# Performance work log

Hardware: AMD Instinct MI355X
Metric: run time of the kernel (lower is better)

The kernel has to match this reference:

```python
import jax, jax.numpy as jnp
import numpy as np

BS, DIM, N_CLASSES = 4096, 512, 100
POS_W, NEG_W = 2.0, 40.0
MARGIN, POS_T, NEG_T = 0.1, 0.5, 0.5


def setup_inputs() -> dict:
    key = jax.random.key(0)
    k1, k2 = jax.random.split(key)
    x = jax.random.normal(k1, (BS, DIM), dtype=jnp.float32)
    x = x / jnp.linalg.norm(x, axis=-1, keepdims=True)  # cosine-mode embeddings
    labels = jax.random.randint(k2, (BS,), 0, N_CLASSES, dtype=jnp.int64 if jax.config.jax_enable_x64 else jnp.int32)
    return {"batch": x, "labels": labels}


def _masked_logsumexp(sims, mask, use_max):
    # Faithful port of Criterion.masked_logsumexp with dim=0 (per-column).
    m = sims * mask  # bool mask promotes; masked-out entries become 0
    ref = jnp.max(m, axis=0) if use_max else jnp.min(m, axis=0)  # (BS,)
    ref = jax.lax.stop_gradient(ref)
    nz = (jnp.max(m, axis=0) + jnp.min(m, axis=0)) != 0  # columns with any nonzero masked entry
    s = jnp.sum(jnp.exp(sims - ref[None, :]) * mask, axis=0)  # (BS,)
    vals = jnp.log(jnp.where(nz, s, 1.0)) + ref
    return vals, nz


def _masked_mean_softplus(vals, nz, w):
    cnt = jnp.sum(nz).astype(vals.dtype)
    sp = jax.nn.softplus(vals) / w
    mean = jnp.sum(jnp.where(nz, sp, 0.0)) / jnp.maximum(cnt, 1.0)
    # torch path returns scalar 0 from masked_logsumexp when no nz columns -> softplus(0)/w
    return jnp.where(cnt > 0, mean, jax.nn.softplus(0.0) / w)


def reference(batch, labels):
    sim = batch @ batch.T                                  # (BS, BS) cosine similarity
    same = labels[:, None] == labels[None, :]
    diff = ~same
    eye = jnp.eye(sim.shape[0], dtype=bool)

    # per-row bounds: hardest positive (min sim, excl. self) / hardest negative (max sim)
    pos_bound = jnp.min(jnp.where(same & ~eye, sim, jnp.inf), axis=1)   # (BS,)
    neg_bound = jnp.max(jnp.where(diff, sim, -jnp.inf), axis=1)        # (BS,)

    # torch broadcasting applies bounds per-COLUMN (last dim)
    neg_mask = diff & (sim + MARGIN > pos_bound[None, :])
    pos_mask = same & (sim - MARGIN < neg_bound[None, :])

    w_pos = -POS_W * (sim - POS_T)
    w_neg = NEG_W * (sim - NEG_T)

    pos_vals, pos_nz = _masked_logsumexp(w_pos, pos_mask, use_max=False)
    neg_vals, neg_nz = _masked_logsumexp(w_neg, neg_mask, use_max=True)

    loss = _masked_mean_softplus(pos_vals, pos_nz, POS_W) \
         + _masked_mean_softplus(neg_vals, neg_nz, NEG_W)
    return loss
```

## Files before the change

### kernel.cpp

```cpp
#include <hip/hip_runtime.h>
#include <stdint.h>


#define BS 4096
#define DIM 512
#define NTILES 528

typedef __attribute__((ext_vector_type(8))) short short8;
typedef __attribute__((ext_vector_type(4))) float f32x4;

#define TILE_USH (128 * 64)

__device__ __forceinline__ unsigned fenc(float f){
  unsigned u = __float_as_uint(f);
  return (u & 0x80000000u) ? ~u : (u | 0x80000000u);
}
__device__ __forceinline__ float fdec(unsigned e){
  unsigned u = (e & 0x80000000u) ? (e & 0x7fffffffu) : ~e;
  return __uint_as_float(u);
}
__device__ __forceinline__ ushort f2bf(float f){
  unsigned u = __float_as_uint(f);
  return (ushort)((u + 0x7fffu + ((u >> 16) & 1u)) >> 16);
}
__device__ __forceinline__ void gld_lds16(void* ldsp, const void* gp){
  __builtin_amdgcn_global_load_lds((const __attribute__((address_space(1))) void*)gp,
                                   (__attribute__((address_space(3))) void*)ldsp, 16, 0, 0);
}

__global__ void k_convert(const float* __restrict__ x, ushort* __restrict__ xh){
  int i = blockIdx.x * blockDim.x + threadIdx.x;
  float4 v = ((const float4*)x)[i];
  ((ushort4*)xh)[i] = make_ushort4(f2bf(v.x), f2bf(v.y), f2bf(v.z), f2bf(v.w));
}

__device__ __forceinline__ void gemm_tile(f32x4 (&acc)[4][4], ushort* lds,
                                          const ushort* __restrict__ Xh,
                                          int Rm, int Rn, int t)
{
  const int l  = t & 63;
  const int w  = t >> 6;
  const int wm = w >> 1, wn = w & 1;
  const int lc = l & 15;
  const int lq = l >> 4;
  const int r0 = t >> 3;
  const int gx = (t & 7) ^ (r0 & 7);
  const int lds_i = t * 8;

  #pragma unroll
  for (int i = 0; i < 4; ++i)
    #pragma unroll
    for (int j = 0; j < 4; ++j) acc[i][j] = (f32x4){0.f, 0.f, 0.f, 0.f};

  for (int ks = 0; ks < 8; ++ks){
    const int kb = ks * 64 + gx * 8;
    #pragma unroll
    for (int rep = 0; rep < 4; ++rep){
      const int row = rep * 32 + r0;
      const int lo  = rep * 2048 + lds_i;
      gld_lds16(&lds[lo],            Xh + (size_t)(Rm + row) * DIM + kb);
      gld_lds16(&lds[TILE_USH + lo], Xh + (size_t)(Rn + row) * DIM + kb);
    }
    __syncthreads();
    #pragma unroll
    for (int kk = 0; kk < 2; ++kk){
      const int gr = kk * 4 + lq;
      const int sl = (gr ^ (l & 7)) * 8;
      short8 ah[4], bh[4];
      #pragma unroll
      for (int f = 0; f < 4; ++f){
        ah[f] = *(const short8*)&lds[(wm * 64 + f * 16 + lc) * 64 + sl];
        bh[f] = *(const short8*)&lds[TILE_USH + (wn * 64 + f * 16 + lc) * 64 + sl];
      }
      #pragma unroll
      for (int fm = 0; fm < 4; ++fm)
        #pragma unroll
        for (int fn = 0; fn < 4; ++fn)
          acc[fm][fn] = __builtin_amdgcn_mfma_f32_16x16x32_bf16(ah[fm], bh[fn], acc[fm][fn], 0, 0, 0);
    }
    __syncthreads();
  }
}

__device__ __forceinline__ void epi_bounds(const f32x4 (&acc)[4][4],
    const int* __restrict__ labels, const int (&labr)[4][4],
    unsigned* pos_enc, unsigned* neg_enc,
    int Rm, int Rn, bool diag, int t)
{
  const int l  = t & 63;
  const int w  = t >> 6;
  const int wm = w >> 1, wn = w & 1;
  const int lc = l & 15, lq = l >> 4;
  const int crow0 = Rm + wm * 64;
  const int ccol0 = Rn + wn * 64;
  const float INF = __builtin_inff();

  #pragma unroll
  for (int fm = 0; fm < 4; ++fm){
    float mn[4] = {INF, INF, INF, INF};
    float mx[4] = {-INF, -INF, -INF, -INF};
    #pragma unroll
    for (int fn = 0; fn < 4; ++fn){
      const int gc = ccol0 + fn * 16 + lc;
      const int labc = labels[gc];
      #pragma unroll
      for (int v = 0; v < 4; ++v){
        const float s = acc[fm][fn][v];
        const int grow = crow0 + fm * 16 + lq * 4 + v;
        const bool same = (labc == labr[fm][v]);
        mn[v] = fminf(mn[v], (same && (grow != gc)) ? s : INF);
        mx[v] = fmaxf(mx[v], same ? -INF : s);
      }
    }
    #pragma unroll
    for (int off = 1; off < 16; off <<= 1)
      #pragma unroll
      for (int v = 0; v < 4; ++v){
        mn[v] = fminf(mn[v], __shfl_xor(mn[v], off));
        mx[v] = fmaxf(mx[v], __shfl_xor(mx[v], off));
      }
    if (lc == 0){
      #pragma unroll
      for (int v = 0; v < 4; ++v){
        const int grow = crow0 + fm * 16 + lq * 4 + v;
        if (mn[v] < INF)  atomicMin(&pos_enc[grow], fenc(mn[v]));
        if (mx[v] > -INF) atomicMax(&neg_enc[grow], fenc(mx[v]));
      }
    }
  }
  if (!diag){
    #pragma unroll
    for (int fn = 0; fn < 4; ++fn){
      const int gc = ccol0 + fn * 16 + lc;
      const int labc = labels[gc];
      float mn = INF, mx = -INF;
      #pragma unroll
      for (int fm = 0; fm < 4; ++fm)
        #pragma unroll
        for (int v = 0; v < 4; ++v){
          const float s = acc[fm][fn][v];
          const bool same = (labc == labr[fm][v]);
          mn = fminf(mn, same ? s : INF);
          mx = fmaxf(mx, same ? -INF : s);
        }
      #pragma unroll
      for (int off = 16; off < 64; off <<= 1){
        mn = fminf(mn, __shfl_xor(mn, off));
        mx = fmaxf(mx, __shfl_xor(mx, off));
      }
      if (l < 16){
        if (mn < INF)  atomicMin(&pos_enc[gc], fenc(mn));
        if (mx > -INF) atomicMax(&neg_enc[gc], fenc(mx));
      }
    }
  }
}

template<bool AB>
__device__ __forceinline__ unsigned rd_enc(unsigned* p){
  if (AB) return __hip_atomic_load(p, __ATOMIC_RELAXED, __HIP_MEMORY_SCOPE_AGENT);
  return *p;
}

template<bool AB>
__device__ __forceinline__ void epi_stats(const f32x4 (&acc)[4][4],
    const int* __restrict__ labels, const int (&labr)[4][4],
    unsigned* pos_enc, unsigned* neg_enc,
    unsigned* maxN_enc, unsigned* minN_enc, float* SN,
    unsigned* maxP_enc, unsigned* minP_enc, float* SP,
    int Rm, int Rn, bool diag, int t)
{
  const int l  = t & 63;
  const int w  = t >> 6;
  const int wm = w >> 1, wn = w & 1;
  const int lc = l & 15, lq = l >> 4;
  const int crow0 = Rm + wm * 64;
  const int ccol0 = Rn + wn * 64;
  const float INF = __builtin_inff();

  #pragma unroll
  for (int fn = 0; fn < 4; ++fn){
    const int gc = ccol0 + fn * 16 + lc;
    const int labc = labels[gc];
    const unsigned pe = rd_enc<AB>(&pos_enc[gc]);
    const float pb = (pe == 0xFFFFFFFFu) ? INF : fdec(pe);
    const unsigned ne = rd_enc<AB>(&neg_enc[gc]);
    const float nb = (ne == 0u) ? -INF : fdec(ne);
    float mxN = -INF, mnN = INF, sN = 0.f;
    float mxP = -INF, mnP = INF, sP = 0.f;
    #pragma unroll
    for (int fm = 0; fm < 4; ++fm)
      #pragma unroll
      for (int v = 0; v < 4; ++v){
        const float s = acc[fm][fn][v];
        const bool same = (labc == labr[fm][v]);
        const float wN = 40.0f * (s - 0.5f);
        const bool mN = (!same) && (s + 0.1f > pb);
        const float mvN = mN ? wN : 0.0f;
        mxN = fmaxf(mxN, mvN); mnN = fminf(mnN, mvN);
        sN += mN ? __expf(wN) : 0.0f;
        const float wP = -2.0f * (s - 0.5f);
        const bool mP = same && (s - 0.1f < nb);
        const float mvP = mP ? wP : 0.0f;
        mxP = fmaxf(mxP, mvP); mnP = fminf(mnP, mvP);
        sP += mP ? __expf(wP) : 0.0f;
      }
    #pragma unroll
    for (int off = 16; off < 64; off <<= 1){
      mxN = fmaxf(mxN, __shfl_xor(mxN, off));
      mnN = fminf(mnN, __shfl_xor(mnN, off));
      sN += __shfl_xor(sN, off);
      mxP = fmaxf(mxP, __shfl_xor(mxP, off));
      mnP = fminf(mnP, __shfl_xor(mnP, off));
      sP += __shfl_xor(sP, off);
    }
    if (l < 16){
      atomicMax(&maxN_enc[gc], fenc(mxN));
      atomicMin(&minN_enc[gc], fenc(mnN));
      atomicAdd(&SN[gc], sN);
      atomicMax(&maxP_enc[gc], fenc(mxP));
      atomicMin(&minP_enc[gc], fenc(mnP));
      atomicAdd(&SP[gc], sP);
    }
  }
  if (!diag){
    #pragma unroll
    for (int fm = 0; fm < 4; ++fm){
      float pbr[4], nbr[4];
      #pragma unroll
      for (int v = 0; v < 4; ++v){
        const int grow = crow0 + fm * 16 + lq * 4 + v;
        const unsigned pe = rd_enc<AB>(&pos_enc[grow]);
        pbr[v] = (pe == 0xFFFFFFFFu) ? INF : fdec(pe);
        const unsigned ne = rd_enc<AB>(&neg_enc[grow]);
        nbr[v] = (ne == 0u) ? -INF : fdec(ne);
      }
      float mxN[4], mnN[4], sN[4], mxP[4], mnP[4], sP[4];
      #pragma unroll
      for (int v = 0; v < 4; ++v){
        mxN[v] = -INF; mnN[v] = INF; sN[v] = 0.f;
        mxP[v] = -INF; mnP[v] = INF; sP[v] = 0.f;
      }
      #pragma unroll
      for (int fn = 0; fn < 4; ++fn){
        const int gc = ccol0 + fn * 16 + lc;
        const int labc = labels[gc];
        #pragma unroll
        for (int v = 0; v < 4; ++v){
          const float s = acc[fm][fn][v];
          const bool same = (labc == labr[fm][v]);
          const float wN = 40.0f * (s - 0.5f);
          const bool mN = (!same) && (s + 0.1f > pbr[v]);
          const float mvN = mN ? wN : 0.0f;
          mxN[v] = fmaxf(mxN[v], mvN); mnN[v] = fminf(mnN[v], mvN);
          sN[v] += mN ? __expf(wN) : 0.0f;
          const float wP = -2.0f * (s - 0.5f);
          const bool mP = same && (s - 0.1f < nbr[v]);
          const float mvP = mP ? wP : 0.0f;
          mxP[v] = fmaxf(mxP[v], mvP); mnP[v] = fminf(mnP[v], mvP);
          sP[v] += mP ? __expf(wP) : 0.0f;
        }
      }
      #pragma unroll
      for (int off = 1; off < 16; off <<= 1)
        #pragma unroll
        for (int v = 0; v < 4; ++v){
          mxN[v] = fmaxf(mxN[v], __shfl_xor(mxN[v], off));
          mnN[v] = fminf(mnN[v], __shfl_xor(mnN[v], off));
          sN[v] += __shfl_xor(sN[v], off);
          mxP[v] = fmaxf(mxP[v], __shfl_xor(mxP[v], off));
          mnP[v] = fminf(mnP[v], __shfl_xor(mnP[v], off));
          sP[v] += __shfl_xor(sP[v], off);
        }
      if (lc == 0){
        #pragma unroll
        for (int v = 0; v < 4; ++v){
          const int grow = crow0 + fm * 16 + lq * 4 + v;
          atomicMax(&maxN_enc[grow], fenc(mxN[v]));
          atomicMin(&minN_enc[grow], fenc(mnN[v]));
          atomicAdd(&SN[grow], sN[v]);
          atomicMax(&maxP_enc[grow], fenc(mxP[v]));
          atomicMin(&minP_enc[grow], fenc(mnP[v]));
          atomicAdd(&SP[grow], sP[v]);
        }
      }
    }
  }
}

__device__ __forceinline__ void decode_tile(int bid, int& Rm, int& Rn, bool& diag){
  int wg = (bid & 7) * 66 + (bid >> 3);
  int ii = wg, bm = 0;
  while (ii >= 32 - bm){ ii -= 32 - bm; ++bm; }
  const int bn = bm + ii;
  diag = (bm == bn);
  Rm = bm * 128; Rn = bn * 128;
}

__global__ __launch_bounds__(256, 3)
void k_fused(const ushort* __restrict__ Xh, const int* __restrict__ labels,
             unsigned* pos_enc, unsigned* neg_enc,
             unsigned* maxN_enc, unsigned* minN_enc, float* SN,
             unsigned* maxP_enc, unsigned* minP_enc, float* SP,
             unsigned* bar)
{
  __shared__ ushort lds[2 * TILE_USH];
  const int t = threadIdx.x;
  int Rm, Rn; bool diag;
  decode_tile((int)blockIdx.x, Rm, Rn, diag);

  f32x4 acc[4][4];
  gemm_tile(acc, lds, Xh, Rm, Rn, t);

  const int wm = (t >> 6) >> 1, lq = (t & 63) >> 4;
  int labr[4][4];
  #pragma unroll
  for (int fm = 0; fm < 4; ++fm)
    #pragma unroll
    for (int v = 0; v < 4; ++v)
      labr[fm][v] = labels[Rm + wm * 64 + fm * 16 + lq * 4 + v];

  epi_bounds(acc, labels, labr, pos_enc, neg_enc, Rm, Rn, diag, t);

  __syncthreads();
  if (t == 0){
    __threadfence();
    __hip_atomic_fetch_add(bar, 1u, __ATOMIC_ACQ_REL, __HIP_MEMORY_SCOPE_AGENT);
    unsigned spins = 0;
    while (__hip_atomic_load(bar, __ATOMIC_ACQUIRE, __HIP_MEMORY_SCOPE_AGENT) < (unsigned)NTILES
           && ++spins < 20000000u)
      __builtin_amdgcn_s_sleep(8);
  }
  __syncthreads();

  epi_stats<true>(acc, labels, labr, pos_enc, neg_enc,
                  maxN_enc, minN_enc, SN, maxP_enc, minP_enc, SP, Rm, Rn, diag, t);
}

template<int PHASE>
__global__ __launch_bounds__(256)
void k_gemm(const ushort* __restrict__ Xh, const int* __restrict__ labels,
            unsigned* pos_enc, unsigned* neg_enc,
            unsigned* maxN_enc, unsigned* minN_enc, float* SN,
            unsigned* maxP_enc, unsigned* minP_enc, float* SP)
{
  __shared__ ushort lds[2 * TILE_USH];
  const int t = threadIdx.x;
  int Rm, Rn; bool diag;
  decode_tile((int)blockIdx.x, Rm, Rn, diag);

  f32x4 acc[4][4];
  gemm_tile(acc, lds, Xh, Rm, Rn, t);

  const int wm = (t >> 6) >> 1, lq = (t & 63) >> 4;
  int labr[4][4];
  #pragma unroll
  for (int fm = 0; fm < 4; ++fm)
    #pragma unroll
    for (int v = 0; v < 4; ++v)
      labr[fm][v] = labels[Rm + wm * 64 + fm * 16 + lq * 4 + v];

  if (PHASE == 1)
    epi_bounds(acc, labels, labr, pos_enc, neg_enc, Rm, Rn, diag, t);
  else
    epi_stats<false>(acc, labels, labr, pos_enc, neg_enc,
                     maxN_enc, minN_enc, SN, maxP_enc, minP_enc, SP, Rm, Rn, diag, t);
}

__global__ void k_finalize(const unsigned* __restrict__ maxN_enc, const unsigned* __restrict__ minN_enc,
                           const float* __restrict__ SN,
                           const unsigned* __restrict__ maxP_enc, const unsigned* __restrict__ minP_enc,
                           const float* __restrict__ SP, float* __restrict__ out)
{
  const int t = threadIdx.x;
  float sumP = 0.f, cP = 0.f, sumN = 0.f, cN = 0.f;
  #pragma unroll
  for (int i = 0; i < 4; ++i){
    const int c = t + i * 1024;
    const float mxN = fdec(maxN_enc[c]), mnN = fdec(minN_enc[c]);
    if (mxN + mnN != 0.0f){ sumN += log1pf(SN[c]); cN += 1.0f; }
    const float mxP = fdec(maxP_enc[c]), mnP = fdec(minP_enc[c]);
    if (mxP + mnP != 0.0f){ sumP += log1pf(SP[c]); cP += 1.0f; }
  }
  #pragma unroll
  for (int off = 32; off; off >>= 1){
    sumP += __shfl_down(sumP, off); cP += __shfl_down(cP, off);
    sumN += __shfl_down(sumN, off); cN += __shfl_down(cN, off);
  }
  __shared__ float red[16][4];
  const int w = t >> 6;
  if ((t & 63) == 0){ red[w][0] = sumP; red[w][1] = cP; red[w][2] = sumN; red[w][3] = cN; }
  __syncthreads();
  if (t == 0){
    float SPs = 0.f, CPs = 0.f, SNs = 0.f, CNs = 0.f;
    for (int i = 0; i < 16; ++i){ SPs += red[i][0]; CPs += red[i][1]; SNs += red[i][2]; CNs += red[i][3]; }
    const float LN2 = 0.69314718055994531f;
    const float tP = (CPs > 0.f) ? (SPs / 2.0f)  / fmaxf(CPs, 1.f) : LN2 / 2.0f;
    const float tN = (CNs > 0.f) ? (SNs / 40.0f) / fmaxf(CNs, 1.f) : LN2 / 40.0f;
    out[0] = tP + tN;
  }
}

extern "C" void kernel_launch(void* const* d_in, const int* in_sizes, int n_in,
                              void* d_out, int out_size, void* d_ws, size_t ws_size,
                              hipStream_t stream) {
  const float* x    = (const float*)d_in[0];
  const int* labels = (const int*)d_in[1];
  char* W = (char*)d_ws;
  ushort* Xh = (ushort*)W;
  char* Z = W + (4u << 20);
  unsigned* neg_enc  = (unsigned*)(Z + 0 * 16384);
  unsigned* maxN_enc = (unsigned*)(Z + 1 * 16384);
  unsigned* maxP_enc = (unsigned*)(Z + 2 * 16384);
  float*    SN       = (float*)   (Z + 3 * 16384);
  float*    SP       = (float*)   (Z + 4 * 16384);
  unsigned* bar      = (unsigned*)(Z + 5 * 16384);
  char* F = Z + 6 * 16384;
  unsigned* pos_enc  = (unsigned*)(F + 0 * 16384);
  unsigned* minN_enc = (unsigned*)(F + 1 * 16384);
  unsigned* minP_enc = (unsigned*)(F + 2 * 16384);

  hipMemsetAsync(Z, 0x00, 6 * 16384, stream);
  hipMemsetAsync(F, 0xFF, 3 * 16384, stream);
  k_convert<<<(BS * DIM / 4) / 256, 256, 0, stream>>>(x, Xh);

  int nb = 0, ncu = 0;
  hipDeviceProp_t prop;
  int dev = 0;
  hipGetDevice(&dev);
  if (hipGetDeviceProperties(&prop, dev) == hipSuccess) ncu = prop.multiProcessorCount;
  bool fused = (hipOccupancyMaxActiveBlocksPerMultiprocessor(&nb, k_fused, 256, 0) == hipSuccess)
               && (ncu > 0) && ((long)nb * ncu >= NTILES);

  if (fused){
    k_fused<<<NTILES, 256, 0, stream>>>(Xh, labels, pos_enc, neg_enc,
                                        maxN_enc, minN_enc, SN, maxP_enc, minP_enc, SP, bar);
  } else {
    k_gemm<1><<<NTILES, 256, 0, stream>>>(Xh, labels, pos_enc, neg_enc,
                                          maxN_enc, minN_enc, SN, maxP_enc, minP_enc, SP);
    k_gemm<2><<<NTILES, 256, 0, stream>>>(Xh, labels, pos_enc, neg_enc,
                                          maxN_enc, minN_enc, SN, maxP_enc, minP_enc, SP);
  }
  k_finalize<<<1, 1024, 0, stream>>>(maxN_enc, minN_enc, SN, maxP_enc, minP_enc, SP, (float*)d_out);
}
```

Baseline: 185.6 us.

## Replace atomics and grid barrier with per-tile partial buffers and separate reduction kernels

```diff
diff --git a/kernel.cpp b/kernel.cpp
--- a/kernel.cpp
+++ b/kernel.cpp
@@ -5,20 +5,13 @@
 #define BS 4096
 #define DIM 512
 #define NTILES 528
+#define NSLOT 32
 
 typedef __attribute__((ext_vector_type(8))) short short8;
 typedef __attribute__((ext_vector_type(4))) float f32x4;
 
 #define TILE_USH (128 * 64)
 
-__device__ __forceinline__ unsigned fenc(float f){
-  unsigned u = __float_as_uint(f);
-  return (u & 0x80000000u) ? ~u : (u | 0x80000000u);
-}
-__device__ __forceinline__ float fdec(unsigned e){
-  unsigned u = (e & 0x80000000u) ? (e & 0x7fffffffu) : ~e;
-  return __uint_as_float(u);
-}
 __device__ __forceinline__ ushort f2bf(float f){
   unsigned u = __float_as_uint(f);
   return (ushort)((u + 0x7fffu + ((u >> 16) & 1u)) >> 16);
@@ -32,6 +25,15 @@
   int i = blockIdx.x * blockDim.x + threadIdx.x;
   float4 v = ((const float4*)x)[i];
   ((ushort4*)xh)[i] = make_ushort4(f2bf(v.x), f2bf(v.y), f2bf(v.z), f2bf(v.w));
+}
+
+__device__ __forceinline__ void decode_tile(int bid, int& Rm, int& Rn, bool& diag){
+  int wg = (bid & 7) * 66 + (bid >> 3);
+  int ii = wg, bm = 0;
+  while (ii >= 32 - bm){ ii -= 32 - bm; ++bm; }
+  const int bn = bm + ii;
+  diag = (bm == bn);
+  Rm = bm * 128; Rn = bn * 128;
 }
 
 __device__ __forceinline__ void gemm_tile(f32x4 (&acc)[4][4], ushort* lds,
@@ -82,18 +84,36 @@
   }
 }
 
-__device__ __forceinline__ void epi_bounds(const f32x4 (&acc)[4][4],
-    const int* __restrict__ labels, const int (&labr)[4][4],
-    unsigned* pos_enc, unsigned* neg_enc,
-    int Rm, int Rn, bool diag, int t)
+__global__ __launch_bounds__(256)
+void k_bounds(const ushort* __restrict__ Xh, const int* __restrict__ labels,
+              float* __restrict__ posB, float* __restrict__ negB)
 {
+  __shared__ ushort lds[2 * TILE_USH];
+  const int t = threadIdx.x;
+  int Rm, Rn; bool diag;
+  decode_tile((int)blockIdx.x, Rm, Rn, diag);
+  const int bm = Rm >> 7, bn = Rn >> 7;
+
+  f32x4 acc[4][4];
+  gemm_tile(acc, lds, Xh, Rm, Rn, t);
+
   const int l  = t & 63;
   const int w  = t >> 6;
   const int wm = w >> 1, wn = w & 1;
   const int lc = l & 15, lq = l >> 4;
-  const int crow0 = Rm + wm * 64;
-  const int ccol0 = Rn + wn * 64;
   const float INF = __builtin_inff();
+
+  int labr[4][4];
+  #pragma unroll
+  for (int fm = 0; fm < 4; ++fm)
+    #pragma unroll
+    for (int v = 0; v < 4; ++v)
+      labr[fm][v] = labels[Rm + wm * 64 + fm * 16 + lq * 4 + v];
+
+  float* sMnS = (float*)lds;
+  float* sMxS = sMnS + 256;
+  float* sMnT = sMnS + 512;
+  float* sMxT = sMnS + 768;
 
   #pragma unroll
   for (int fm = 0; fm < 4; ++fm){
@@ -101,12 +121,12 @@
     float mx[4] = {-INF, -INF, -INF, -INF};
     #pragma unroll
     for (int fn = 0; fn < 4; ++fn){
-      const int gc = ccol0 + fn * 16 + lc;
+      const int gc = Rn + wn * 64 + fn * 16 + lc;
       const int labc = labels[gc];
       #pragma unroll
       for (int v = 0; v < 4; ++v){
         const float s = acc[fm][fn][v];
-        const int grow = crow0 + fm * 16 + lq * 4 + v;
+        const int grow = Rm + wm * 64 + fm * 16 + lq * 4 + v;
         const bool same = (labc == labr[fm][v]);
         mn[v] = fminf(mn[v], (same && (grow != gc)) ? s : INF);
         mx[v] = fmaxf(mx[v], same ? -INF : s);
@@ -122,16 +142,16 @@
     if (lc == 0){
       #pragma unroll
       for (int v = 0; v < 4; ++v){
-        const int grow = crow0 + fm * 16 + lq * 4 + v;
-        if (mn[v] < INF)  atomicMin(&pos_enc[grow], fenc(mn[v]));
-        if (mx[v] > -INF) atomicMax(&neg_enc[grow], fenc(mx[v]));
+        const int r64 = fm * 16 + lq * 4 + v;
+        sMnS[(wm * 2 + wn) * 64 + r64] = mn[v];
+        sMxS[(wm * 2 + wn) * 64 + r64] = mx[v];
       }
     }
   }
   if (!diag){
     #pragma unroll
     for (int fn = 0; fn < 4; ++fn){
-      const int gc = ccol0 + fn * 16 + lc;
+      const int gc = Rn + wn * 64 + fn * 16 + lc;
       const int labc = labels[gc];
       float mn = INF, mx = -INF;
       #pragma unroll
@@ -149,170 +169,56 @@
         mx = fmaxf(mx, __shfl_xor(mx, off));
       }
       if (l < 16){
-        if (mn < INF)  atomicMin(&pos_enc[gc], fenc(mn));
-        if (mx > -INF) atomicMax(&neg_enc[gc], fenc(mx));
-      }
-    }
-  }
-}
-
-template<bool AB>
-__device__ __forceinline__ unsigned rd_enc(unsigned* p){
-  if (AB) return __hip_atomic_load(p, __ATOMIC_RELAXED, __HIP_MEMORY_SCOPE_AGENT);
-  return *p;
-}
-
-template<bool AB>
-__device__ __forceinline__ void epi_stats(const f32x4 (&acc)[4][4],
-    const int* __restrict__ labels, const int (&labr)[4][4],
-    unsigned* pos_enc, unsigned* neg_enc,
-    unsigned* maxN_enc, unsigned* minN_enc, float* SN,
-    unsigned* maxP_enc, unsigned* minP_enc, float* SP,
-    int Rm, int Rn, bool diag, int t)
-{
-  const int l  = t & 63;
-  const int w  = t >> 6;
-  const int wm = w >> 1, wn = w & 1;
-  const int lc = l & 15, lq = l >> 4;
-  const int crow0 = Rm + wm * 64;
-  const int ccol0 = Rn + wn * 64;
-  const float INF = __builtin_inff();
-
-  #pragma unroll
-  for (int fn = 0; fn < 4; ++fn){
-    const int gc = ccol0 + fn * 16 + lc;
-    const int labc = labels[gc];
-    const unsigned pe = rd_enc<AB>(&pos_enc[gc]);
-    const float pb = (pe == 0xFFFFFFFFu) ? INF : fdec(pe);
-    const unsigned ne = rd_enc<AB>(&neg_enc[gc]);
-    const float nb = (ne == 0u) ? -INF : fdec(ne);
-    float mxN = -INF, mnN = INF, sN = 0.f;
-    float mxP = -INF, mnP = INF, sP = 0.f;
-    #pragma unroll
-    for (int fm = 0; fm < 4; ++fm)
-      #pragma unroll
-      for (int v = 0; v < 4; ++v){
-        const float s = acc[fm][fn][v];
-        const bool same = (labc == labr[fm][v]);
-        const float wN = 40.0f * (s - 0.5f);
-        const bool mN = (!same) && (s + 0.1f > pb);
-        const float mvN = mN ? wN : 0.0f;
-        mxN = fmaxf(mxN, mvN); mnN = fminf(mnN, mvN);
-        sN += mN ? __expf(wN) : 0.0f;
-        const float wP = -2.0f * (s - 0.5f);
-        const bool mP = same && (s - 0.1f < nb);
-        const float mvP = mP ? wP : 0.0f;
-        mxP = fmaxf(mxP, mvP); mnP = fminf(mnP, mvP);
-        sP += mP ? __expf(wP) : 0.0f;
-      }
-    #pragma unroll
-    for (int off = 16; off < 64; off <<= 1){
-      mxN = fmaxf(mxN, __shfl_xor(mxN, off));
-      mnN = fminf(mnN, __shfl_xor(mnN, off));
-      sN += __shfl_xor(sN, off);
-      mxP = fmaxf(mxP, __shfl_xor(mxP, off));
-      mnP = fminf(mnP, __shfl_xor(mnP, off));
-      sP += __shfl_xor(sP, off);
-    }
-    if (l < 16){
-      atomicMax(&maxN_enc[gc], fenc(mxN));
-      atomicMin(&minN_enc[gc], fenc(mnN));
-      atomicAdd(&SN[gc], sN);
-      atomicMax(&maxP_enc[gc], fenc(mxP));
-      atomicMin(&minP_enc[gc], fenc(mnP));
-      atomicAdd(&SP[gc], sP);
-    }
-  }
-  if (!diag){
-    #pragma unroll
-    for (int fm = 0; fm < 4; ++fm){
-      float pbr[4], nbr[4];
-      #pragma unroll
-      for (int v = 0; v < 4; ++v){
-        const int grow = crow0 + fm * 16 + lq * 4 + v;
-        const unsigned pe = rd_enc<AB>(&pos_enc[grow]);
-        pbr[v] = (pe == 0xFFFFFFFFu) ? INF : fdec(pe);
-        const unsigned ne = rd_enc<AB>(&neg_enc[grow]);
-        nbr[v] = (ne == 0u) ? -INF : fdec(ne);
-      }
-      float mxN[4], mnN[4], sN[4], mxP[4], mnP[4], sP[4];
-      #pragma unroll
-      for (int v = 0; v < 4; ++v){
-        mxN[v] = -INF; mnN[v] = INF; sN[v] = 0.f;
-        mxP[v] = -INF; mnP[v] = INF; sP[v] = 0.f;
-      }
-      #pragma unroll
-      for (int fn = 0; fn < 4; ++fn){
-        const int gc = ccol0 + fn * 16 + lc;
-        const int labc = labels[gc];
-        #pragma unroll
-        for (int v = 0; v < 4; ++v){
-          const float s = acc[fm][fn][v];
-          const bool same = (labc == labr[fm][v]);
-          const float wN = 40.0f * (s - 0.5f);
-          const bool mN = (!same) && (s + 0.1f > pbr[v]);
-          const float mvN = mN ? wN : 0.0f;
-          mxN[v] = fmaxf(mxN[v], mvN); mnN[v] = fminf(mnN[v], mvN);
-          sN[v] += mN ? __expf(wN) : 0.0f;
-          const float wP = -2.0f * (s - 0.5f);
-          const bool mP = same && (s - 0.1f < nbr[v]);
-          const float mvP = mP ? wP : 0.0f;
-          mxP[v] = fmaxf(mxP[v], mvP); mnP[v] = fminf(mnP[v], mvP);
-          sP[v] += mP ? __expf(wP) : 0.0f;
-        }
-      }
-      #pragma unroll
-      for (int off = 1; off < 16; off <<= 1)
-        #pragma unroll
-        for (int v = 0; v < 4; ++v){
-          mxN[v] = fmaxf(mxN[v], __shfl_xor(mxN[v], off));
-          mnN[v] = fminf(mnN[v], __shfl_xor(mnN[v], off));
-          sN[v] += __shfl_xor(sN[v], off);
-          mxP[v] = fmaxf(mxP[v], __shfl_xor(mxP[v], off));
-          mnP[v] = fminf(mnP[v], __shfl_xor(mnP[v], off));
-          sP[v] += __shfl_xor(sP[v], off);
-        }
-      if (lc == 0){
-        #pragma unroll
-        for (int v = 0; v < 4; ++v){
-          const int grow = crow0 + fm * 16 + lq * 4 + v;
-          atomicMax(&maxN_enc[grow], fenc(mxN[v]));
-          atomicMin(&minN_enc[grow], fenc(mnN[v]));
-          atomicAdd(&SN[grow], sN[v]);
-          atomicMax(&maxP_enc[grow], fenc(mxP[v]));
-          atomicMin(&minP_enc[grow], fenc(mnP[v]));
-          atomicAdd(&SP[grow], sP[v]);
-        }
-      }
-    }
-  }
-}
-
-__device__ __forceinline__ void decode_tile(int bid, int& Rm, int& Rn, bool& diag){
-  int wg = (bid & 7) * 66 + (bid >> 3);
-  int ii = wg, bm = 0;
-  while (ii >= 32 - bm){ ii -= 32 - bm; ++bm; }
-  const int bn = bm + ii;
-  diag = (bm == bn);
-  Rm = bm * 128; Rn = bn * 128;
-}
-
-__global__ __launch_bounds__(256, 3)
-void k_fused(const ushort* __restrict__ Xh, const int* __restrict__ labels,
-             unsigned* pos_enc, unsigned* neg_enc,
-             unsigned* maxN_enc, unsigned* minN_enc, float* SN,
-             unsigned* maxP_enc, unsigned* minP_enc, float* SP,
-             unsigned* bar)
+        const int c64 = fn * 16 + lc;
+        sMnT[(wn * 2 + wm) * 64 + c64] = mn;
+        sMxT[(wn * 2 + wm) * 64 + c64] = mx;
+      }
+    }
+  }
+  __syncthreads();
+  if (t < 128){
+    const int h = t >> 6, r = t & 63;
+    posB[(size_t)bn * BS + Rm + t] = fminf(sMnS[(h * 2 + 0) * 64 + r], sMnS[(h * 2 + 1) * 64 + r]);
+    negB[(size_t)bn * BS + Rm + t] = fmaxf(sMxS[(h * 2 + 0) * 64 + r], sMxS[(h * 2 + 1) * 64 + r]);
+    if (!diag){
+      posB[(size_t)bm * BS + Rn + t] = fminf(sMnT[(h * 2 + 0) * 64 + r], sMnT[(h * 2 + 1) * 64 + r]);
+      negB[(size_t)bm * BS + Rn + t] = fmaxf(sMxT[(h * 2 + 0) * 64 + r], sMxT[(h * 2 + 1) * 64 + r]);
+    }
+  }
+}
+
+__global__ void k_redbounds(const float* __restrict__ posB, const float* __restrict__ negB,
+                            float* __restrict__ pos_bound, float* __restrict__ neg_bound){
+  const int r = blockIdx.x * 256 + threadIdx.x;
+  float mn = __builtin_inff(), mx = -__builtin_inff();
+  #pragma unroll
+  for (int s = 0; s < NSLOT; ++s){
+    mn = fminf(mn, posB[(size_t)s * BS + r]);
+    mx = fmaxf(mx, negB[(size_t)s * BS + r]);
+  }
+  pos_bound[r] = mn;
+  neg_bound[r] = mx;
+}
+
+__global__ __launch_bounds__(256)
+void k_stats(const ushort* __restrict__ Xh, const int* __restrict__ labels,
+             const float* __restrict__ pos_bound, const float* __restrict__ neg_bound,
+             float* __restrict__ SNp, float* __restrict__ SPp)
 {
   __shared__ ushort lds[2 * TILE_USH];
   const int t = threadIdx.x;
   int Rm, Rn; bool diag;
   decode_tile((int)blockIdx.x, Rm, Rn, diag);
+  const int bm = Rm >> 7, bn = Rn >> 7;
 
   f32x4 acc[4][4];
   gemm_tile(acc, lds, Xh, Rm, Rn, t);
 
-  const int wm = (t >> 6) >> 1, lq = (t & 63) >> 4;
+  const int l  = t & 63;
+  const int w  = t >> 6;
+  const int wm = w >> 1, wn = w & 1;
+  const int lc = l & 15, lq = l >> 4;
+
   int labr[4][4];
   #pragma unroll
   for (int fm = 0; fm < 4; ++fm)
@@ -320,67 +226,106 @@
     for (int v = 0; v < 4; ++v)
       labr[fm][v] = labels[Rm + wm * 64 + fm * 16 + lq * 4 + v];
 
-  epi_bounds(acc, labels, labr, pos_enc, neg_enc, Rm, Rn, diag, t);
-
+  float* sSNs = (float*)lds;
+  float* sSPs = sSNs + 256;
+  float* sSNt = sSNs + 512;
+  float* sSPt = sSNs + 768;
+
+  #pragma unroll
+  for (int fn = 0; fn < 4; ++fn){
+    const int gc = Rn + wn * 64 + fn * 16 + lc;
+    const int labc = labels[gc];
+    const float pb = pos_bound[gc];
+    const float nb = neg_bound[gc];
+    float sN = 0.f, sP = 0.f;
+    #pragma unroll
+    for (int fm = 0; fm < 4; ++fm)
+      #pragma unroll
+      for (int v = 0; v < 4; ++v){
+        const float s = acc[fm][fn][v];
+        const bool same = (labc == labr[fm][v]);
+        sN += ((!same) && (s + 0.1f > pb)) ? __expf(40.0f * (s - 0.5f)) : 0.0f;
+        sP += (same && (s - 0.1f < nb))    ? __expf(-2.0f * (s - 0.5f)) : 0.0f;
+      }
+    #pragma unroll
+    for (int off = 16; off < 64; off <<= 1){
+      sN += __shfl_xor(sN, off);
+      sP += __shfl_xor(sP, off);
+    }
+    if (l < 16){
+      const int c64 = fn * 16 + lc;
+      sSNs[(wn * 2 + wm) * 64 + c64] = sN;
+      sSPs[(wn * 2 + wm) * 64 + c64] = sP;
+    }
+  }
+  if (!diag){
+    #pragma unroll
+    for (int fm = 0; fm < 4; ++fm){
+      float pbr[4], nbr[4];
+      #pragma unroll
+      for (int v = 0; v < 4; ++v){
+        const int grow = Rm + wm * 64 + fm * 16 + lq * 4 + v;
+        pbr[v] = pos_bound[grow];
+        nbr[v] = neg_bound[grow];
+      }
+      float sN[4] = {0.f, 0.f, 0.f, 0.f}, sP[4] = {0.f, 0.f, 0.f, 0.f};
+      #pragma unroll
+      for (int fn = 0; fn < 4; ++fn){
+        const int gc = Rn + wn * 64 + fn * 16 + lc;
+        const int labc = labels[gc];
+        #pragma unroll
+        for (int v = 0; v < 4; ++v){
+          const float s = acc[fm][fn][v];
+          const bool same = (labc == labr[fm][v]);
+          sN[v] += ((!same) && (s + 0.1f > pbr[v])) ? __expf(40.0f * (s - 0.5f)) : 0.0f;
+          sP[v] += (same && (s - 0.1f < nbr[v]))    ? __expf(-2.0f * (s - 0.5f)) : 0.0f;
+        }
+      }
+      #pragma unroll
+      for (int off = 1; off < 16; off <<= 1)
+        #pragma unroll
+        for (int v = 0; v < 4; ++v){
+          sN[v] += __shfl_xor(sN[v], off);
+          sP[v] += __shfl_xor(sP[v], off);
+        }
+      if (lc == 0){
+        #pragma unroll
+        for (int v = 0; v < 4; ++v){
+          const int r64 = fm * 16 + lq * 4 + v;
+          sSNt[(wm * 2 + wn) * 64 + r64] = sN[v];
+          sSPt[(wm * 2 + wn) * 64 + r64] = sP[v];
+        }
+      }
+    }
+  }
   __syncthreads();
-  if (t == 0){
-    __threadfence();
-    __hip_atomic_fetch_add(bar, 1u, __ATOMIC_ACQ_REL, __HIP_MEMORY_SCOPE_AGENT);
-    unsigned spins = 0;
-    while (__hip_atomic_load(bar, __ATOMIC_ACQUIRE, __HIP_MEMORY_SCOPE_AGENT) < (unsigned)NTILES
-           && ++spins < 20000000u)
-      __builtin_amdgcn_s_sleep(8);
-  }
-  __syncthreads();
-
-  epi_stats<true>(acc, labels, labr, pos_enc, neg_enc,
-                  maxN_enc, minN_enc, SN, maxP_enc, minP_enc, SP, Rm, Rn, diag, t);
-}
-
-template<int PHASE>
-__global__ __launch_bounds__(256)
-void k_gemm(const ushort* __restrict__ Xh, const int* __restrict__ labels,
-            unsigned* pos_enc, unsigned* neg_enc,
-            unsigned* maxN_enc, unsigned* minN_enc, float* SN,
-            unsigned* maxP_enc, unsigned* minP_enc, float* SP)
-{
-  __shared__ ushort lds[2 * TILE_USH];
-  const int t = threadIdx.x;
-  int Rm, Rn; bool diag;
-  decode_tile((int)blockIdx.x, Rm, Rn, diag);
-
-  f32x4 acc[4][4];
-  gemm_tile(acc, lds, Xh, Rm, Rn, t);
-
-  const int wm = (t >> 6) >> 1, lq = (t & 63) >> 4;
-  int labr[4][4];
-  #pragma unroll
-  for (int fm = 0; fm < 4; ++fm)
-    #pragma unroll
-    for (int v = 0; v < 4; ++v)
-      labr[fm][v] = labels[Rm + wm * 64 + fm * 16 + lq * 4 + v];
-
-  if (PHASE == 1)
-    epi_bounds(acc, labels, labr, pos_enc, neg_enc, Rm, Rn, diag, t);
-  else
-    epi_stats<false>(acc, labels, labr, pos_enc, neg_enc,
-                     maxN_enc, minN_enc, SN, maxP_enc, minP_enc, SP, Rm, Rn, diag, t);
-}
-
-__global__ void k_finalize(const unsigned* __restrict__ maxN_enc, const unsigned* __restrict__ minN_enc,
-                           const float* __restrict__ SN,
-                           const unsigned* __restrict__ maxP_enc, const unsigned* __restrict__ minP_enc,
-                           const float* __restrict__ SP, float* __restrict__ out)
+  if (t < 128){
+    const int h = t >> 6, r = t & 63;
+    SNp[(size_t)bm * BS + Rn + t] = sSNs[(h * 2 + 0) * 64 + r] + sSNs[(h * 2 + 1) * 64 + r];
+    SPp[(size_t)bm * BS + Rn + t] = sSPs[(h * 2 + 0) * 64 + r] + sSPs[(h * 2 + 1) * 64 + r];
+    if (!diag){
+      SNp[(size_t)bn * BS + Rm + t] = sSNt[(h * 2 + 0) * 64 + r] + sSNt[(h * 2 + 1) * 64 + r];
+      SPp[(size_t)bn * BS + Rm + t] = sSPt[(h * 2 + 0) * 64 + r] + sSPt[(h * 2 + 1) * 64 + r];
+    }
+  }
+}
+
+__global__ void k_finalize(const float* __restrict__ SNp, const float* __restrict__ SPp,
+                           float* __restrict__ out)
 {
   const int t = threadIdx.x;
   float sumP = 0.f, cP = 0.f, sumN = 0.f, cN = 0.f;
   #pragma unroll
   for (int i = 0; i < 4; ++i){
     const int c = t + i * 1024;
-    const float mxN = fdec(maxN_enc[c]), mnN = fdec(minN_enc[c]);
-    if (mxN + mnN != 0.0f){ sumN += log1pf(SN[c]); cN += 1.0f; }
-    const float mxP = fdec(maxP_enc[c]), mnP = fdec(minP_enc[c]);
-    if (mxP + mnP != 0.0f){ sumP += log1pf(SP[c]); cP += 1.0f; }
+    float sn = 0.f, sp = 0.f;
+    #pragma unroll
+    for (int s = 0; s < NSLOT; ++s){
+      sn += SNp[(size_t)s * BS + c];
+      sp += SPp[(size_t)s * BS + c];
+    }
+    if (sn != 0.0f){ sumN += log1pf(sn); cN += 1.0f; }
+    if (sp != 0.0f){ sumP += log1pf(sp); cP += 1.0f; }
   }
   #pragma unroll
   for (int off = 32; off; off >>= 1){
@@ -407,39 +352,15 @@
   const float* x    = (const float*)d_in[0];
   const int* labels = (const int*)d_in[1];
   char* W = (char*)d_ws;
-  ushort* Xh = (ushort*)W;
-  char* Z = W + (4u << 20);
-  unsigned* neg_enc  = (unsigned*)(Z + 0 * 16384);
-  unsigned* maxN_enc = (unsigned*)(Z + 1 * 16384);
-  unsigned* maxP_enc = (unsigned*)(Z + 2 * 16384);
-  float*    SN       = (float*)   (Z + 3 * 16384);
-  float*    SP       = (float*)   (Z + 4 * 16384);
-  unsigned* bar      = (unsigned*)(Z + 5 * 16384);
-  char* F = Z + 6 * 16384;
-  unsigned* pos_enc  = (unsigned*)(F + 0 * 16384);
-  unsigned* minN_enc = (unsigned*)(F + 1 * 16384);
-  unsigned* minP_enc = (unsigned*)(F + 2 * 16384);
-
-  hipMemsetAsync(Z, 0x00, 6 * 16384, stream);
-  hipMemsetAsync(F, 0xFF, 3 * 16384, stream);
+  ushort* Xh        = (ushort*)W;
+  float*  P1        = (float*)(W + (4u << 20));
+  float*  P2        = (float*)(W + (4u << 20) + (512u << 10));
+  float*  pos_bound = (float*)(W + (5u << 20));
+  float*  neg_bound = (float*)(W + (5u << 20) + (16u << 10));
+
   k_convert<<<(BS * DIM / 4) / 256, 256, 0, stream>>>(x, Xh);
-
-  int nb = 0, ncu = 0;
-  hipDeviceProp_t prop;
-  int dev = 0;
-  hipGetDevice(&dev);
-  if (hipGetDeviceProperties(&prop, dev) == hipSuccess) ncu = prop.multiProcessorCount;
-  bool fused = (hipOccupancyMaxActiveBlocksPerMultiprocessor(&nb, k_fused, 256, 0) == hipSuccess)
-               && (ncu > 0) && ((long)nb * ncu >= NTILES);
-
-  if (fused){
-    k_fused<<<NTILES, 256, 0, stream>>>(Xh, labels, pos_enc, neg_enc,
-                                        maxN_enc, minN_enc, SN, maxP_enc, minP_enc, SP, bar);
-  } else {
-    k_gemm<1><<<NTILES, 256, 0, stream>>>(Xh, labels, pos_enc, neg_enc,
-                                          maxN_enc, minN_enc, SN, maxP_enc, minP_enc, SP);
-    k_gemm<2><<<NTILES, 256, 0, stream>>>(Xh, labels, pos_enc, neg_enc,
-                                          maxN_enc, minN_enc, SN, maxP_enc, minP_enc, SP);
-  }
-  k_finalize<<<1, 1024, 0, stream>>>(maxN_enc, minN_enc, SN, maxP_enc, minP_enc, SP, (float*)d_out);
-}
+  k_bounds<<<NTILES, 256, 0, stream>>>(Xh, labels, P1, P2);
+  k_redbounds<<<BS / 256, 256, 0, stream>>>(P1, P2, pos_bound, neg_bound);
+  k_stats<<<NTILES, 256, 0, stream>>>(Xh, labels, pos_bound, neg_bound, P1, P2);
+  k_finalize<<<1, 1024, 0, stream>>>(P1, P2, (float*)d_out);
+}
```

Measured after the change: 179.4 us. -3.3%, faster.
